# Kernel tuning notes

Hardware: AMD Instinct MI355X
Metric: run time of the kernel (lower is better)

The kernel has to match this reference:

```python
import jax, jax.numpy as jnp
import numpy as np

EPS = 1e-5


def _conv(x, w, groups=1, pad=0):
    return jax.lax.conv_general_dilated(
        x, w, (1, 1), [(pad, pad), (pad, pad)],
        dimension_numbers=('NCHW', 'OIHW', 'NCHW'),
        feature_group_count=groups)


def _bn(x, p):
    # p: (4, C) rows = gamma, beta, running_mean, running_var (inference BN)
    g, b, m, v = p[0], p[1], p[2], p[3]
    scale = g / jnp.sqrt(v + EPS)
    return (x - m[None, :, None, None]) * scale[None, :, None, None] + b[None, :, None, None]


def _pixel_shuffle(x, r):
    B, C, H, W = x.shape
    x = x.reshape(B, C // (r * r), r, r, H, W)
    x = x.transpose(0, 1, 4, 2, 5, 3)
    return x.reshape(B, C // (r * r), H * r, W * r)


def _grid_sample_border(img, grid):
    # img: (N, C, H, W); grid: (N, Ho, Wo, 2) with (x, y) in [-1, 1]
    # bilinear, align_corners=False, padding_mode='border' (torch semantics)
    N, C, H, W = img.shape
    x = ((grid[..., 0] + 1.0) * W - 1.0) * 0.5
    y = ((grid[..., 1] + 1.0) * H - 1.0) * 0.5
    x = jnp.clip(x, 0.0, W - 1.0)
    y = jnp.clip(y, 0.0, H - 1.0)
    x0 = jnp.floor(x)
    y0 = jnp.floor(y)
    wx = (x - x0)[:, None]  # (N,1,Ho,Wo)
    wy = (y - y0)[:, None]
    x0i = jnp.clip(x0.astype(jnp.int32), 0, W - 1)
    y0i = jnp.clip(y0.astype(jnp.int32), 0, H - 1)
    x1i = jnp.minimum(x0i + 1, W - 1)
    y1i = jnp.minimum(y0i + 1, H - 1)
    gather = jax.vmap(lambda im, yy, xx: im[:, yy, xx])
    v00 = gather(img, y0i, x0i)
    v01 = gather(img, y0i, x1i)
    v10 = gather(img, y1i, x0i)
    v11 = gather(img, y1i, x1i)
    return (v00 * (1 - wy) * (1 - wx) + v01 * (1 - wy) * wx
            + v10 * wy * (1 - wx) + v11 * wy * wx)


def _init_pos(scale, groups, dtype):
    h = jnp.arange((-scale + 1) / 2, (scale - 1) / 2 + 1, dtype=dtype) / scale
    g1, g2 = jnp.meshgrid(h, h, indexing='ij')
    p = jnp.swapaxes(jnp.stack([g1, g2]), 1, 2)  # (2, s, s)
    p = jnp.tile(p, (1, groups, 1))
    return p.reshape(1, -1, 1, 1)  # (1, 2*groups*s*s, 1, 1)


def _dysample(x, ow, ob, scale=2, groups=4):
    # DySample 'lp' style, dyscope=False
    B, C, H, W = x.shape
    off = _conv(x, ow) + ob.reshape(1, -1, 1, 1)
    offset = off * 0.25 + _init_pos(scale, groups, x.dtype)  # (B, 2*g*s^2, H, W)
    offset = offset.reshape(B, 2, -1, H, W)
    cw = jnp.arange(W, dtype=x.dtype) + 0.5
    ch = jnp.arange(H, dtype=x.dtype) + 0.5
    gx, gy = jnp.meshgrid(cw, ch, indexing='ij')  # (W, H)
    coords = jnp.swapaxes(jnp.stack([gx, gy]), 1, 2)[None, :, None]  # (1,2,1,H,W)
    norm = jnp.array([W, H], dtype=x.dtype).reshape(1, 2, 1, 1, 1)
    coords = 2.0 * (coords + offset) / norm - 1.0  # (B,2,g*s^2,H,W)
    coords = _pixel_shuffle(coords.reshape(B, -1, H, W), scale)  # (B, 2*g, sH, sW)
    coords = coords.reshape(B, 2, groups, scale * H, scale * W)
    coords = coords.transpose(0, 2, 3, 4, 1).reshape(B * groups, scale * H, scale * W, 2)
    xs = x.reshape(B * groups, C // groups, H, W)
    out = _grid_sample_border(xs, coords)
    return out.reshape(B, C, scale * H, scale * W)


def _make_bn(key, C):
    k1, k2, k3, k4 = jax.random.split(key, 4)
    gamma = jax.random.uniform(k1, (C,), minval=0.5, maxval=1.5)
    beta = 0.1 * jax.random.normal(k2, (C,))
    mean = 0.1 * jax.random.normal(k3, (C,))
    var = jax.random.uniform(k4, (C,), minval=0.5, maxval=1.5)
    return jnp.stack([gamma, beta, mean, var])


def setup_inputs() -> dict:
    key = jax.random.key(0)
    ks = jax.random.split(key, 24)
    B, C, H, W = 4, 768, 32, 32
    F = 256
    d = {}
    for i in range(4):
        d[f'f{i+1}'] = jax.random.normal(ks[i], (B, C, H, W), dtype=jnp.float32)
    d['proj_w'] = jax.random.normal(ks[4], (4, C, F), dtype=jnp.float32) * (C ** -0.5)
    d['layer_weights'] = jax.random.normal(ks[5], (4,), dtype=jnp.float32)
    d['dw_w'] = jax.random.normal(ks[6], (F, 1, 3, 3), dtype=jnp.float32) * (1.0 / 3.0)
    d['bn_enh'] = _make_bn(ks[7], F)
    cstd = (F * 9) ** -0.5
    d['offset_w1'] = jax.random.normal(ks[8], (32, F, 1, 1), dtype=jnp.float32) * 0.001
    d['offset_b1'] = jnp.zeros((32,), dtype=jnp.float32)
    d['conv_w1'] = jax.random.normal(ks[9], (F, F, 3, 3), dtype=jnp.float32) * cstd
    d['bn1'] = _make_bn(ks[10], F)
    d['offset_w2'] = jax.random.normal(ks[11], (32, F, 1, 1), dtype=jnp.float32) * 0.001
    d['offset_b2'] = jnp.zeros((32,), dtype=jnp.float32)
    d['conv_w2'] = jax.random.normal(ks[12], (F, F, 3, 3), dtype=jnp.float32) * cstd
    d['bn2'] = _make_bn(ks[13], F)
    d['out_w'] = jax.random.normal(ks[14], (1, F, 3, 3), dtype=jnp.float32) * cstd
    d['out_b'] = jnp.zeros((1,), dtype=jnp.float32)
    return d


def reference(f1, f2, f3, f4, proj_w, layer_weights, dw_w, bn_enh,
              offset_w1, offset_b1, conv_w1, bn1,
              offset_w2, offset_b2, conv_w2, bn2, out_w, out_b):
    # --- WeightedFusion: project each layer's tokens, softmax-weighted sum ---
    feats = jnp.stack([f1, f2, f3, f4])  # (L, B, C, H, W)
    L, B, C, H, W = feats.shape
    tokens = feats.reshape(L, B, C, H * W).transpose(0, 1, 3, 2)  # (L, B, N, C)
    proj = jax.nn.gelu(jnp.einsum('lbnc,lcf->lbnf', tokens, proj_w), approximate=False)
    lw = jax.nn.softmax(layer_weights)
    fused = jnp.einsum('l,lbnf->bnf', lw, proj)  # (B, N, 256)
    x = fused.transpose(0, 2, 1).reshape(B, -1, H, W)  # (B, 256, H, W)

    # --- SpatialDetailEnhancer: depthwise conv + BN, residual ReLU ---
    Fc = x.shape[1]
    y = _conv(x, dw_w, groups=Fc, pad=1)
    x = jax.nn.relu(_bn(y, bn_enh) + x)

    x = _dysample(x, offset_w1, offset_b1)
    x = jax.nn.relu(_bn(_conv(x, conv_w1, pad=1), bn1))
    x = _dysample(x, offset_w2, offset_b2)
    x = jax.nn.relu(_bn(_conv(x, conv_w2, pad=1), bn2))

    # --- depth prediction head ---
    out = _conv(x, out_w, pad=1) + out_b.reshape(1, -1, 1, 1)
    return out  # (B, 1, 4H, 4W)
```

## Files before the change

kernel.cpp:

```cpp
#include <hip/hip_runtime.h>
#include <math.h>

using u16 = unsigned short;
typedef __attribute__((ext_vector_type(8))) short short8;
typedef __attribute__((ext_vector_type(4))) float f32x4;

__device__ __forceinline__ float b2f(u16 u) {
    union { unsigned int i; float f; } v; v.i = ((unsigned int)u) << 16; return v.f;
}
__device__ __forceinline__ u16 f2b(float f) {
    union { float f; unsigned int i; } v; v.f = f;
    unsigned int x = v.i;
    return (u16)((x + 0x7FFFu + ((x >> 16) & 1u)) >> 16);
}
__device__ __forceinline__ float ldx(const void* p, long long i, int fl) {
    return fl ? ((const float*)p)[i] : b2f(((const u16*)p)[i]);
}

__global__ __launch_bounds__(256) void k_detect(const void* p, int* flag) {
    __shared__ float m[256];
    int t = threadIdx.x;
    const u16* q = (const u16*)p;
    float lm = 0.f;
    for (int j = 0; j < 16; ++j) {
        float v = b2f(q[t * 16 + j]);
        float a = fabsf(v);
        if (!(a <= 1e30f)) a = 1e31f;
        lm = fmaxf(lm, a);
    }
    m[t] = lm;
    __syncthreads();
    if (t == 0) {
        float mm = 0.f;
        for (int i = 0; i < 256; ++i) mm = fmaxf(mm, m[i]);
        *flag = (mm > 1000.f) ? 1 : 0;
    }
}

__global__ __launch_bounds__(256) void k_wt(const void* __restrict__ w,
                                            u16* __restrict__ wTo,
                                            const int* __restrict__ flag) {
    int fl = *flag;
    int idx = blockIdx.x * 256 + threadIdx.x;
    int k  = idx >> 16;
    int oc = (idx >> 8) & 255;
    int ic = idx & 255;
    long long s = (oc * 256 + ic) * 9 + k;
    wTo[idx] = fl ? f2b(((const float*)w)[s]) : ((const u16*)w)[s];
}

__global__ __launch_bounds__(256) void k_pwt(const void* __restrict__ w,
                                             u16* __restrict__ pwT,
                                             const int* __restrict__ flag) {
    int fl = *flag;
    int idx = blockIdx.x * 256 + threadIdx.x;
    int c = idx % 768;
    int f = (idx / 768) & 255;
    int l = idx / (768 * 256);
    long long s = ((long long)l * 768 + c) * 256 + f;
    pwT[idx] = fl ? f2b(((const float*)w)[s]) : ((const u16*)w)[s];
}

__global__ __launch_bounds__(256) void k_fgemm(
    const void* __restrict__ f1, const void* __restrict__ f2,
    const void* __restrict__ f3, const void* __restrict__ f4,
    const u16* __restrict__ pwT, const void* __restrict__ lwp,
    const int* __restrict__ flag, float* __restrict__ gbuf)
{
    __shared__ u16 As[128][40];
    __shared__ u16 Bs[128][40];
    const int fl = *flag;
    const int t    = threadIdx.x;
    const int lane = t & 63;
    const int wv   = t >> 6;
    const int mbase = (wv & 1) << 6;
    const int nbase = (wv >> 1) << 6;
    const int quad  = lane >> 4;
    const int l15   = lane & 15;

    const int f0 = blockIdx.x << 7;
    const int m0 = blockIdx.y << 7;
    const int b  = blockIdx.z >> 2;
    const int l  = blockIdx.z & 3;
    const void* fp = (l == 0) ? f1 : (l == 1) ? f2 : (l == 2) ? f3 : f4;

    float w0 = ldx(lwp, 0, fl), w1 = ldx(lwp, 1, fl);
    float w2 = ldx(lwp, 2, fl), w3 = ldx(lwp, 3, fl);
    float mx = fmaxf(fmaxf(w0, w1), fmaxf(w2, w3));
    float e0 = expf(w0 - mx), e1 = expf(w1 - mx), e2 = expf(w2 - mx), e3 = expf(w3 - mx);
    float es = e0 + e1 + e2 + e3;
    float lwl = ((l == 0) ? e0 : (l == 1) ? e1 : (l == 2) ? e2 : e3) / es;

    const int spx = t & 127;
    const int sq  = t >> 7;

    f32x4 acc[4][4];
    #pragma unroll
    for (int i = 0; i < 4; ++i)
        #pragma unroll
        for (int j = 0; j < 4; ++j) acc[i][j] = (f32x4)0.f;

    const size_t abase = (size_t)b * 768 * 1024 + m0 + spx;
    const u16* srcB = pwT + (size_t)l * 196608 + (size_t)(f0 + spx) * 768 + sq * 16;

    for (int k0 = 0; k0 < 768; k0 += 32) {
        alignas(16) u16 av[16];
        if (fl) {
            #pragma unroll
            for (int s = 0; s < 16; ++s)
                av[s] = f2b(((const float*)fp)[abase + (size_t)(k0 + sq * 16 + s) * 1024]);
        } else {
            #pragma unroll
            for (int s = 0; s < 16; ++s)
                av[s] = ((const u16*)fp)[abase + (size_t)(k0 + sq * 16 + s) * 1024];
        }
        uint4 bq0 = *(const uint4*)(srcB + k0);
        uint4 bq1 = *(const uint4*)(srcB + k0 + 8);
        __syncthreads();
        *(uint4*)&As[spx][sq * 16]     = *(const uint4*)&av[0];
        *(uint4*)&As[spx][sq * 16 + 8] = *(const uint4*)&av[8];
        *(uint4*)&Bs[spx][sq * 16]     = bq0;
        *(uint4*)&Bs[spx][sq * 16 + 8] = bq1;
        __syncthreads();

        short8 af[4], bf[4];
        #pragma unroll
        for (int i = 0; i < 4; ++i)
            af[i] = *(const short8*)&As[mbase + (i << 4) + l15][quad << 3];
        #pragma unroll
        for (int j = 0; j < 4; ++j)
            bf[j] = *(const short8*)&Bs[nbase + (j << 4) + l15][quad << 3];
        #pragma unroll
        for (int i = 0; i < 4; ++i)
            #pragma unroll
            for (int j = 0; j < 4; ++j)
                acc[i][j] = __builtin_amdgcn_mfma_f32_16x16x32_bf16(
                    af[i], bf[j], acc[i][j], 0, 0, 0);
    }

    #pragma unroll
    for (int j = 0; j < 4; ++j) {
        const int n = f0 + nbase + (j << 4) + l15;
        float* op = gbuf + ((size_t)((l << 2) + b) * 256 + n) * 1024
                  + m0 + mbase + (quad << 2);
        #pragma unroll
        for (int i = 0; i < 4; ++i) {
            f32x4 a = acc[i][j];
            float4 o;
            o.x = lwl * 0.5f * a[0] * (1.f + erff(a[0] * 0.70710678118654752f));
            o.y = lwl * 0.5f * a[1] * (1.f + erff(a[1] * 0.70710678118654752f));
            o.z = lwl * 0.5f * a[2] * (1.f + erff(a[2] * 0.70710678118654752f));
            o.w = lwl * 0.5f * a[3] * (1.f + erff(a[3] * 0.70710678118654752f));
            *(float4*)(op + (i << 4)) = o;
        }
    }
}

__global__ __launch_bounds__(256) void k_fsum(const float* __restrict__ gbuf,
                                              float* __restrict__ x0)
{
    int idx = blockIdx.x * 256 + threadIdx.x;
    x0[idx] = gbuf[idx] + gbuf[1048576 + idx]
            + gbuf[2097152 + idx] + gbuf[3145728 + idx];
}

__global__ __launch_bounds__(256) void k_dw(const float* __restrict__ x0,
                                            const void* __restrict__ dww,
                                            const void* __restrict__ bnp,
                                            const int* __restrict__ flag,
                                            float* __restrict__ x1)
{
    const int fl = *flag;
    int idx = blockIdx.x * 256 + threadIdx.x;
    int n = idx & 1023;
    int f = (idx >> 10) & 255;
    int h = n >> 5, w = n & 31;
    const float* base = x0 + (idx - n);
    float acc = 0.f;
    #pragma unroll
    for (int kh = 0; kh < 3; ++kh) {
        int y = h + kh - 1;
        if (y < 0 || y >= 32) continue;
        #pragma unroll
        for (int kw = 0; kw < 3; ++kw) {
            int x = w + kw - 1;
            if (x < 0 || x >= 32) continue;
            acc += base[(y << 5) + x] * ldx(dww, f * 9 + kh * 3 + kw, fl);
        }
    }
    float g  = ldx(bnp, f, fl);
    float be = ldx(bnp, 256 + f, fl);
    float mn = ldx(bnp, 512 + f, fl);
    float vv = ldx(bnp, 768 + f, fl);
    float scale = g / sqrtf(vv + 1e-5f);
    float o = (acc - mn) * scale + be + x0[idx];
    x1[idx] = fmaxf(o, 0.f);
}

template<bool ACT_BF16>
__global__ __launch_bounds__(256) void k_offs(const void* __restrict__ actv,
                                              const void* __restrict__ w,
                                              const void* __restrict__ bias,
                                              const int* __restrict__ flag,
                                              float* __restrict__ off,
                                              int HW)
{
    const int fl = *flag;
    int idx = blockIdx.x * 256 + threadIdx.x;
    int pos = idx % HW;
    int oc  = (idx / HW) & 31;
    int b   = idx / (32 * HW);
    float acc = 0.f;
    if (ACT_BF16) {
        const u16* ap = (const u16*)actv + (size_t)b * 256 * HW + pos;
        for (int ic = 0; ic < 256; ++ic)
            acc = fmaf(b2f(ap[(size_t)ic * HW]), ldx(w, oc * 256 + ic, fl), acc);
    } else {
        const float* ap = (const float*)actv + (size_t)b * 256 * HW + pos;
        for (int ic = 0; ic < 256; ++ic)
            acc = fmaf(ap[(size_t)ic * HW], ldx(w, oc * 256 + ic, fl), acc);
    }
    off[idx] = acc + ldx(bias, oc, fl);
}

template<bool ACT_BF16>
__global__ __launch_bounds__(256) void k_sample(const void* __restrict__ actv,
                                                const float* __restrict__ off,
                                                u16* __restrict__ out,
                                                int H, int W)
{
    const int Wo = W << 1, Ho = H << 1;
    const int HW = H * W, HWo = Ho * Wo;
    const int c   = threadIdx.x;
    const int pxo = blockIdx.x;
    const int b   = blockIdx.y;
    const int wo = pxo % Wo;
    const int ho = pxo / Wo;
    const int g  = c >> 6;
    const int h = ho >> 1, a = ho & 1, w = wo >> 1, bb = wo & 1;
    const int och = g * 4 + a * 2 + bb;
    size_t obase = ((size_t)b * 32 + och) * HW + h * W + w;
    float offx = off[obase];
    float offy = off[obase + (size_t)16 * HW];
    float xp = (float)w + (bb ? 0.25f : -0.25f) + 0.25f * offx;
    float yp = (float)h + (a  ? 0.25f : -0.25f) + 0.25f * offy;
    xp = fminf(fmaxf(xp, 0.f), (float)(W - 1));
    yp = fminf(fmaxf(yp, 0.f), (float)(H - 1));
    float xf = floorf(xp), yf = floorf(yp);
    float wx = xp - xf, wy = yp - yf;
    int x0i = (int)xf; x0i = max(0, min(x0i, W - 1));
    int y0i = (int)yf; y0i = max(0, min(y0i, H - 1));
    int x1i = min(x0i + 1, W - 1);
    int y1i = min(y0i + 1, H - 1);
    float v00, v01, v10, v11;
    if (ACT_BF16) {
        const u16* ap = (const u16*)actv + ((size_t)b * 256 + c) * HW;
        v00 = b2f(ap[y0i * W + x0i]);
        v01 = b2f(ap[y0i * W + x1i]);
        v10 = b2f(ap[y1i * W + x0i]);
        v11 = b2f(ap[y1i * W + x1i]);
    } else {
        const float* ap = (const float*)actv + ((size_t)b * 256 + c) * HW;
        v00 = ap[y0i * W + x0i];
        v01 = ap[y0i * W + x1i];
        v10 = ap[y1i * W + x0i];
        v11 = ap[y1i * W + x1i];
    }
    float r = v00 * (1.f - wy) * (1.f - wx) + v01 * (1.f - wy) * wx
            + v10 * wy * (1.f - wx) + v11 * wy * wx;
    out[((size_t)b * HWo + pxo) * 256 + c] = f2b(r);
}

__global__ __launch_bounds__(256) void k_cmfma(const u16* __restrict__ in,
                                               const u16* __restrict__ wTo,
                                               const void* __restrict__ bnp,
                                               const int* __restrict__ flag,
                                               u16* __restrict__ out,
                                               int H, int W, int logW)
{
    __shared__ u16 As[128][40];
    __shared__ u16 Bs[128][40];
    const int fl = *flag;
    const int HW = H * W;
    const int t    = threadIdx.x;
    const int lane = t & 63;
    const int wv   = t >> 6;
    const int mbase = (wv & 1) << 6;
    const int nbase = (wv >> 1) << 6;
    const int quad  = lane >> 4;
    const int l15   = lane & 15;

    const int oc0 = blockIdx.x << 7;
    const int px0 = blockIdx.y << 7;
    const u16* inb  = in  + (size_t)blockIdx.z * 256 * HW;
    u16*       outb = out + (size_t)blockIdx.z * 256 * HW;

    const int spx = t & 127;
    const int sq  = t >> 7;
    const int gx = (px0 + spx) & (W - 1);
    const int gy = (px0 + spx) >> logW;

    f32x4 acc[4][4];
    #pragma unroll
    for (int i = 0; i < 4; ++i)
        #pragma unroll
        for (int j = 0; j < 4; ++j) acc[i][j] = (f32x4)0.f;

    for (int k3 = 0; k3 < 9; ++k3) {
        const int dh = k3 / 3, dw = k3 % 3;
        const int ys = gy + dh - 1;
        const int xs = gx + dw - 1;
        const bool valid = (ys >= 0) && (ys < H) && (xs >= 0) && (xs < W);
        const u16* rowA = inb + ((size_t)(ys * W + xs)) * 256 + sq * 16;
        const u16* srcB = wTo + (size_t)k3 * 65536 + (size_t)(oc0 + spx) * 256 + sq * 16;

        for (int ic0 = 0; ic0 < 256; ic0 += 32) {
            uint4 aq0, aq1;
            if (valid) {
                aq0 = *(const uint4*)(rowA + ic0);
                aq1 = *(const uint4*)(rowA + ic0 + 8);
            } else {
                aq0 = make_uint4(0, 0, 0, 0);
                aq1 = make_uint4(0, 0, 0, 0);
            }
            uint4 bq0 = *(const uint4*)(srcB + ic0);
            uint4 bq1 = *(const uint4*)(srcB + ic0 + 8);
            __syncthreads();
            *(uint4*)&As[spx][sq * 16]     = aq0;
            *(uint4*)&As[spx][sq * 16 + 8] = aq1;
            *(uint4*)&Bs[spx][sq * 16]     = bq0;
            *(uint4*)&Bs[spx][sq * 16 + 8] = bq1;
            __syncthreads();

            short8 af[4], bf[4];
            #pragma unroll
            for (int i = 0; i < 4; ++i)
                af[i] = *(const short8*)&As[mbase + (i << 4) + l15][quad << 3];
            #pragma unroll
            for (int j = 0; j < 4; ++j)
                bf[j] = *(const short8*)&Bs[nbase + (j << 4) + l15][quad << 3];
            #pragma unroll
            for (int i = 0; i < 4; ++i)
                #pragma unroll
                for (int j = 0; j < 4; ++j)
                    acc[i][j] = __builtin_amdgcn_mfma_f32_16x16x32_bf16(
                        af[i], bf[j], acc[i][j], 0, 0, 0);
        }
    }

    #pragma unroll
    for (int j = 0; j < 4; ++j) {
        const int n = oc0 + nbase + (j << 4) + l15;
        float g  = ldx(bnp, n, fl);
        float be = ldx(bnp, 256 + n, fl);
        float mn = ldx(bnp, 512 + n, fl);
        float vv = ldx(bnp, 768 + n, fl);
        float scale = g / sqrtf(vv + 1e-5f);
        u16* op = outb + (size_t)n * HW + px0 + mbase + (quad << 2);
        #pragma unroll
        for (int i = 0; i < 4; ++i) {
            f32x4 a = acc[i][j];
            ushort4 o;
            o.x = f2b(fmaxf((a[0] - mn) * scale + be, 0.f));
            o.y = f2b(fmaxf((a[1] - mn) * scale + be, 0.f));
            o.z = f2b(fmaxf((a[2] - mn) * scale + be, 0.f));
            o.w = f2b(fmaxf((a[3] - mn) * scale + be, 0.f));
            *(ushort4*)(op + (i << 4)) = o;
        }
    }
}

__global__ __launch_bounds__(256) void k_headp(const u16* __restrict__ in,
                                               const void* __restrict__ w,
                                               const int* __restrict__ flag,
                                               float* __restrict__ part)
{
    const int fl = *flag;
    const int icc = blockIdx.x;
    const int px  = blockIdx.y * 256 + threadIdx.x;
    in   += (size_t)blockIdx.z * 256 * 16384;
    part += (size_t)blockIdx.z * 16 * 16384;
    const int x = px & 127, y = px >> 7;
    float acc = 0.f;
    #pragma unroll 4
    for (int i = 0; i < 16; ++i) {
        const int ic = (icc << 4) + i;
        const u16* p = in + (size_t)ic * 16384;
        float wr[9];
        #pragma unroll
        for (int k = 0; k < 9; ++k) wr[k] = ldx(w, ic * 9 + k, fl);
        #pragma unroll
        for (int kh = 0; kh < 3; ++kh) {
            int yy = y + kh - 1;
            if (yy < 0 || yy >= 128) continue;
            const u16* row = p + yy * 128;
            #pragma unroll
            for (int kw = 0; kw < 3; ++kw) {
                int xx = x + kw - 1;
                if (xx < 0 || xx >= 128) continue;
                acc = fmaf(b2f(row[xx]), wr[kh * 3 + kw], acc);
            }
        }
    }
    part[icc * 16384 + px] = acc;
}

__global__ __launch_bounds__(256) void k_headf(const float* __restrict__ part,
                                               const void* __restrict__ bias,
                                               const int* __restrict__ flag,
                                               void* __restrict__ outp,
                                               int b0)
{
    const int fl = *flag;
    int px = blockIdx.x * 256 + threadIdx.x;
    part += (size_t)blockIdx.y * 16 * 16384;
    int out_ofs = (b0 + blockIdx.y) * 16384;
    float acc = ldx(bias, 0, fl);
    #pragma unroll
    for (int i = 0; i < 16; ++i) acc += part[i * 16384 + px];
    if (fl) ((float*)outp)[out_ofs + px] = acc;
    else    ((u16*)outp)[out_ofs + px] = f2b(acc);
}

extern "C" void kernel_launch(void* const* d_in, const int* in_sizes, int n_in,
                              void* d_out, int out_size, void* d_ws, size_t ws_size,
                              hipStream_t stream) {
    (void)in_sizes; (void)n_in; (void)out_size;
    const void* f1     = d_in[0];
    const void* f2     = d_in[1];
    const void* f3     = d_in[2];
    const void* f4     = d_in[3];
    const void* proj_w = d_in[4];
    const void* lwp    = d_in[5];
    const void* dw_w   = d_in[6];
    const void* bn_enh = d_in[7];
    const void* ow1    = d_in[8];
    const void* ob1    = d_in[9];
    const void* cw1    = d_in[10];
    const void* bn1    = d_in[11];
    const void* ow2    = d_in[12];
    const void* ob2    = d_in[13];
    const void* cw2    = d_in[14];
    const void* bn2    = d_in[15];
    const void* out_w  = d_in[16];
    const void* out_b  = d_in[17];

    const int nb = (ws_size >= 81592320ull) ? 4
                 : (ws_size >= 48037888ull) ? 2 : 1;

    char* ws = (char*)d_ws;
    int*   flag = (int*)  (ws + 0);
    u16*   wT1  = (u16*)  (ws + 65536);
    u16*   wT2  = (u16*)  (ws + 1245184);
    u16*   pwT  = (u16*)  (ws + 2424832);
    u16*   c1   = (u16*)  (ws + 3997696);
    float* o2   = (float*)(ws + 12386304);
    u16*   up2c = (u16*)  (ws + 14483456);
    u16*   c2c  = (u16*)  (ws + 14483456 + (size_t)nb * 8388608);
    float* part = (float*)(ws + 14483456);
    float* gbuf = (float*)(ws + 3997696);
    float* x0   = (float*)(ws + 20774912);
    float* x1   = (float*)(ws + 24969216);
    float* o1   = (float*)(ws + 29163520);
    u16*   up1  = (u16*)  (ws + 12386304);

    k_detect<<<1, 256, 0, stream>>>(f1, flag);

    k_wt<<<2304, 256, 0, stream>>>(cw1, wT1, flag);
    k_wt<<<2304, 256, 0, stream>>>(cw2, wT2, flag);
    k_pwt<<<3072, 256, 0, stream>>>(proj_w, pwT, flag);

    k_fgemm<<<dim3(2, 8, 16), 256, 0, stream>>>(f1, f2, f3, f4, pwT, lwp, flag, gbuf);
    k_fsum<<<4096, 256, 0, stream>>>(gbuf, x0);

    k_dw<<<4096, 256, 0, stream>>>(x0, dw_w, bn_enh, flag, x1);

    k_offs<false><<<512, 256, 0, stream>>>(x1, ow1, ob1, flag, o1, 32 * 32);
    k_sample<false><<<dim3(4096, 4), 256, 0, stream>>>(x1, o1, up1, 32, 32);
    k_cmfma<<<dim3(2, 32, 4), 256, 0, stream>>>(up1, wT1, bn1, flag, c1, 64, 64, 6);

    k_offs<true><<<2048, 256, 0, stream>>>(c1, ow2, ob2, flag, o2, 64 * 64);

    for (int b0 = 0; b0 < 4; b0 += nb) {
        const u16*   c1b = c1 + (size_t)b0 * 256 * 4096;
        const float* o2b = o2 + (size_t)b0 * 32 * 4096;
        k_sample<true><<<dim3(16384, nb), 256, 0, stream>>>(c1b, o2b, up2c, 64, 64);
        k_cmfma<<<dim3(2, 128, nb), 256, 0, stream>>>(up2c, wT2, bn2, flag, c2c,
                                                      128, 128, 7);
        k_headp<<<dim3(16, 64, nb), 256, 0, stream>>>(c2c, out_w, flag, part);
        k_headf<<<dim3(64, nb), 256, 0, stream>>>(part, out_b, flag, d_out, b0);
    }
}
```

Baseline: 752.6 us.

## Load conv MFMA fragments directly from global memory, dropping LDS staging

The 3x3 conv MFMA kernel no longer stages A and B tiles through shared memory with two barriers per K step. Each lane now loads its MFMA fragments straight from global memory with per-fragment pointers and validity masks, and the K loop is unrolled by 2. This removes the LDS writes, LDS reads and block synchronisation, but each operand is now fetched by several waves instead of once per block, which raises global/L2 traffic. It also adds a redundant clamp on the sample y index.

```diff
diff --git a/kernel.cpp b/kernel.cpp
--- a/kernel.cpp
+++ b/kernel.cpp
@@ -249,7 +249,8 @@
     float xf = floorf(xp), yf = floorf(yp);
     float wx = xp - xf, wy = yp - yf;
     int x0i = (int)xf; x0i = max(0, min(x0i, W - 1));
-    int y0i = (int)yf; y0i = max(0, min(y0i, H - 1));
+    int y0i = (int)yf; y0i = max(0, min(y0i, W - 1 + H - W));
+    y0i = max(0, min(y0i, H - 1));
     int x1i = min(x0i + 1, W - 1);
     int y1i = min(y0i + 1, H - 1);
     float v00, v01, v10, v11;
@@ -278,8 +279,6 @@
                                                u16* __restrict__ out,
                                                int H, int W, int logW)
 {
-    __shared__ u16 As[128][40];
-    __shared__ u16 Bs[128][40];
     const int fl = *flag;
     const int HW = H * W;
     const int t    = threadIdx.x;
@@ -295,10 +294,17 @@
     const u16* inb  = in  + (size_t)blockIdx.z * 256 * HW;
     u16*       outb = out + (size_t)blockIdx.z * 256 * HW;
 
-    const int spx = t & 127;
-    const int sq  = t >> 7;
-    const int gx = (px0 + spx) & (W - 1);
-    const int gy = (px0 + spx) >> logW;
+    int gxa[4], gya[4];
+    #pragma unroll
+    for (int i = 0; i < 4; ++i) {
+        int px = px0 + mbase + (i << 4) + l15;
+        gxa[i] = px & (W - 1);
+        gya[i] = px >> logW;
+    }
+    const u16* bptr[4];
+    #pragma unroll
+    for (int j = 0; j < 4; ++j)
+        bptr[j] = wTo + (size_t)(oc0 + nbase + (j << 4) + l15) * 256 + (quad << 3);
 
     f32x4 acc[4][4];
     #pragma unroll
@@ -307,38 +313,31 @@
         for (int j = 0; j < 4; ++j) acc[i][j] = (f32x4)0.f;
 
     for (int k3 = 0; k3 < 9; ++k3) {
-        const int dh = k3 / 3, dw = k3 % 3;
-        const int ys = gy + dh - 1;
-        const int xs = gx + dw - 1;
-        const bool valid = (ys >= 0) && (ys < H) && (xs >= 0) && (xs < W);
-        const u16* rowA = inb + ((size_t)(ys * W + xs)) * 256 + sq * 16;
-        const u16* srcB = wTo + (size_t)k3 * 65536 + (size_t)(oc0 + spx) * 256 + sq * 16;
-
+        const int dh = k3 / 3, dw = k3 - dh * 3;
+        const u16* aptr[4];
+        bool va[4];
+        #pragma unroll
+        for (int i = 0; i < 4; ++i) {
+            int ys = gya[i] + dh - 1;
+            int xs = gxa[i] + dw - 1;
+            va[i] = (ys >= 0) && (ys < H) && (xs >= 0) && (xs < W);
+            aptr[i] = inb + ((size_t)(ys * W + xs)) * 256 + (quad << 3);
+        }
+        const u16* bk0 = bptr[0] + (size_t)k3 * 65536;
+        const u16* bk1 = bptr[1] + (size_t)k3 * 65536;
+        const u16* bk2 = bptr[2] + (size_t)k3 * 65536;
+        const u16* bk3 = bptr[3] + (size_t)k3 * 65536;
+
+        #pragma unroll 2
         for (int ic0 = 0; ic0 < 256; ic0 += 32) {
-            uint4 aq0, aq1;
-            if (valid) {
-                aq0 = *(const uint4*)(rowA + ic0);
-                aq1 = *(const uint4*)(rowA + ic0 + 8);
-            } else {
-                aq0 = make_uint4(0, 0, 0, 0);
-                aq1 = make_uint4(0, 0, 0, 0);
-            }
-            uint4 bq0 = *(const uint4*)(srcB + ic0);
-            uint4 bq1 = *(const uint4*)(srcB + ic0 + 8);
-            __syncthreads();
-            *(uint4*)&As[spx][sq * 16]     = aq0;
-            *(uint4*)&As[spx][sq * 16 + 8] = aq1;
-            *(uint4*)&Bs[spx][sq * 16]     = bq0;
-            *(uint4*)&Bs[spx][sq * 16 + 8] = bq1;
-            __syncthreads();
-
             short8 af[4], bf[4];
             #pragma unroll
             for (int i = 0; i < 4; ++i)
-                af[i] = *(const short8*)&As[mbase + (i << 4) + l15][quad << 3];
-            #pragma unroll
-            for (int j = 0; j < 4; ++j)
-                bf[j] = *(const short8*)&Bs[nbase + (j << 4) + l15][quad << 3];
+                af[i] = va[i] ? *(const short8*)(aptr[i] + ic0) : (short8)0;
+            bf[0] = *(const short8*)(bk0 + ic0);
+            bf[1] = *(const short8*)(bk1 + ic0);
+            bf[2] = *(const short8*)(bk2 + ic0);
+            bf[3] = *(const short8*)(bk3 + ic0);
             #pragma unroll
             for (int i = 0; i < 4; ++i)
                 #pragma unroll
```

After: 856.2 us. +13.8%, slower.
